# Performance work log

Measured on AMD Instinct MI355X. Metric: run time of the kernel, lower is better.

The kernel has to match this reference:

```python
import jax, jax.numpy as jnp
import numpy as np
from math import sqrt

NUM_HEADS = 16
NUM_KV_HEADS = 4
ROPE_BASE = 10000.0


def setup_inputs() -> dict:
    key = jax.random.key(0)
    ks = jax.random.split(key, 9)
    B, S, E = 4, 2048, 2048
    KV_DIM = NUM_KV_HEADS * (E // NUM_HEADS)  # 512
    s = 0.02
    return {
        "x": jax.random.normal(ks[0], (B, S, E), jnp.float32),
        "wq": jax.random.normal(ks[1], (E, E), jnp.float32) * s,
        "bq": jnp.zeros((E,), jnp.float32),
        "wk": jax.random.normal(ks[2], (KV_DIM, E), jnp.float32) * s,
        "bk": jnp.zeros((KV_DIM,), jnp.float32),
        "wv": jax.random.normal(ks[3], (KV_DIM, E), jnp.float32) * s,
        "bv": jnp.zeros((KV_DIM,), jnp.float32),
        "wo": jax.random.normal(ks[4], (E, E), jnp.float32) * s,
        "bo": jnp.zeros((E,), jnp.float32),
    }


def _rope_cos_sin(seq_len, head_dim, dtype):
    inv_freq = 1.0 / (ROPE_BASE ** (jnp.arange(0, head_dim, 2, dtype=jnp.float32) / head_dim))
    pos = jnp.arange(seq_len, dtype=jnp.float32)
    freqs = pos[:, None] * inv_freq[None, :]            # [S, D/2]
    emb = jnp.concatenate([freqs, freqs], axis=-1)      # [S, D]
    return jnp.cos(emb).astype(dtype), jnp.sin(emb).astype(dtype)


def _apply_rope(t, cos, sin):
    # t: [B, H, S, D]; cos/sin: [S, D]
    d2 = t.shape[-1] // 2
    rot = jnp.concatenate([-t[..., d2:], t[..., :d2]], axis=-1)
    return t * cos[None, None, :, :] + rot * sin[None, None, :, :]


def reference(x, wq, bq, wk, bk, wv, bv, wo, bo):
    B, S, E = x.shape
    H, KV = NUM_HEADS, NUM_KV_HEADS
    D = E // H
    G = H // KV

    q = (x @ wq.T + bq).reshape(B, S, H, D).transpose(0, 2, 1, 3)   # [B,H,S,D]
    k = (x @ wk.T + bk).reshape(B, S, KV, D).transpose(0, 2, 1, 3)  # [B,KV,S,D]
    v = (x @ wv.T + bv).reshape(B, S, KV, D).transpose(0, 2, 1, 3)

    cos, sin = _rope_cos_sin(S, D, x.dtype)
    q = _apply_rope(q, cos, sin)
    k = _apply_rope(k, cos, sin)

    # GQA: expand each kv head group_size times (contiguous repeat)
    k = jnp.repeat(k, G, axis=1)  # [B,H,S,D]
    v = jnp.repeat(v, G, axis=1)

    scores = jnp.einsum("bhqd,bhkd->bhqk", q, k)
    causal = jnp.triu(jnp.ones((S, S), dtype=bool), k=1)
    scores = jnp.where(causal[None, None, :, :], -jnp.inf, scores)
    attn = jax.nn.softmax(scores / sqrt(D), axis=-1)
    out = jnp.einsum("bhqk,bhkd->bhqd", attn, v)        # [B,H,S,D]
    out = out.transpose(0, 2, 1, 3).reshape(B, S, E)
    return out @ wo.T + bo
```

## Files before the change

kernel.cpp:

```cpp
#include <hip/hip_runtime.h>
#include <stdint.h>
#include <math.h>

typedef __attribute__((ext_vector_type(8))) short s16x8;
typedef __attribute__((ext_vector_type(4))) short s16x4;
typedef __attribute__((ext_vector_type(4))) float f32x4;

#define NEGH (-1.0e30f)

__device__ __forceinline__ short f2bf(float f) {
  union { float f; unsigned int i; } c; c.f = f;
  unsigned int lsb = (c.i >> 16) & 1u;
  c.i += 0x7fffu + lsb;
  return (short)(c.i >> 16);
}
__device__ __forceinline__ float bf2f(short u) {
  union { unsigned int i; float f; } c;
  c.i = ((unsigned int)(unsigned short)u) << 16;
  return c.f;
}

#define GLOAD_LDS16(gp, lp)                                                  \
  __builtin_amdgcn_global_load_lds(                                          \
      (__attribute__((address_space(1))) void*)(void*)(gp),                  \
      (__attribute__((address_space(3))) void*)(lp), 16, 0, 0)

__global__ __launch_bounds__(256) void cvt_kernel(const float* __restrict__ in,
                                                  short* __restrict__ out)
{
  const size_t i = ((size_t)blockIdx.x * 256 + threadIdx.x) * 4;
  const float4 v = *(const float4*)(in + i);
  s16x4 o = { f2bf(v.x), f2bf(v.y), f2bf(v.z), f2bf(v.w) };
  *(s16x4*)(out + i) = o;
}

__global__ __launch_bounds__(256) void gemm_bt(
    const short* __restrict__ A, const short* __restrict__ W,
    const float* __restrict__ bias, void* __restrict__ C,
    int M, int N, int K, int omode)
{
  __shared__ __align__(16) short As[128 * 64];
  __shared__ __align__(16) short Bs[128 * 64];

  const int t = threadIdx.x;
  const int l = t & 63;
  const int w = t >> 6;
  const int lane16 = l & 15;
  const int quad = l >> 4;
  const int wm = w >> 1, wn = w & 1;
  const int mb0 = blockIdx.y * 128;
  const int nb0 = blockIdx.x * 128;

  const f32x4 zero = {0.f, 0.f, 0.f, 0.f};
  f32x4 acc[4][4];
#pragma unroll
  for (int i = 0; i < 4; ++i)
#pragma unroll
    for (int j = 0; j < 4; ++j) acc[i][j] = zero;

  const int sr = t >> 3;
  const int sp = t & 7;
  const short* Ag = A + (size_t)(mb0 + sr) * K + sp * 8;
  const short* Wg = W + (size_t)(nb0 + sr) * K + sp * 8;
  short* Al = As + t * 8;
  short* Bl = Bs + t * 8;

  const int nkt = K >> 6;
  for (int kt = 0; kt < nkt; ++kt) {
    __syncthreads();
    const int kof = kt * 64;
#pragma unroll
    for (int it = 0; it < 4; ++it) {
      GLOAD_LDS16(Ag + kof + (size_t)(it * 32) * K, Al + it * 2048);
      GLOAD_LDS16(Wg + kof + (size_t)(it * 32) * K, Bl + it * 2048);
    }
    __syncthreads();
#pragma unroll
    for (int kk = 0; kk < 2; ++kk) {
      s16x8 af[4], bf[4];
#pragma unroll
      for (int mi = 0; mi < 4; ++mi)
        af[mi] = *(const s16x8*)&As[(wm * 64 + mi * 16 + lane16) * 64 +
                                    kk * 32 + quad * 8];
#pragma unroll
      for (int ni = 0; ni < 4; ++ni)
        bf[ni] = *(const s16x8*)&Bs[(wn * 64 + ni * 16 + lane16) * 64 +
                                    kk * 32 + quad * 8];
#pragma unroll
      for (int mi = 0; mi < 4; ++mi)
#pragma unroll
        for (int ni = 0; ni < 4; ++ni)
          acc[mi][ni] = __builtin_amdgcn_mfma_f32_16x16x32_bf16(
              af[mi], bf[ni], acc[mi][ni], 0, 0, 0);
    }
  }

#pragma unroll
  for (int ni = 0; ni < 4; ++ni) {
    const int n = nb0 + wn * 64 + ni * 16 + lane16;
    const float bv = bias[n];
#pragma unroll
    for (int mi = 0; mi < 4; ++mi) {
      const int m0 = mb0 + wm * 64 + mi * 16 + quad * 4;
#pragma unroll
      for (int r = 0; r < 4; ++r) {
        const int m = m0 + r;
        const float v = acc[mi][ni][r] + bv;
        if (omode == 0) {
          ((short*)C)[(size_t)m * N + n] = f2bf(v);
        } else if (omode == 1) {
          ((float*)C)[(size_t)m * N + n] = v;
        } else {
          ((short*)C)[((size_t)(m >> 11) * N + n) * 2048 + (m & 2047)] = f2bf(v);
        }
      }
    }
  }
}

__global__ __launch_bounds__(512, 2) void gemm256_bt(
    const short* __restrict__ A, const short* __restrict__ W,
    const float* __restrict__ bias, void* __restrict__ C,
    int M, int N, int K, int omode)
{
  __shared__ __align__(16) short Asm[2 * 16384];
  __shared__ __align__(16) short Bsm[2 * 16384];

  const int t = threadIdx.x;
  const int l = t & 63;
  const int w = t >> 6;
  const int lane16 = l & 15;
  const int quad = l >> 4;
  const int wm = w >> 2;
  const int wn = w & 3;
  const int mb0 = blockIdx.y * 256;
  const int nb0 = blockIdx.x * 256;

  const f32x4 zero = {0.f, 0.f, 0.f, 0.f};
  f32x4 acc[8][4];
#pragma unroll
  for (int i = 0; i < 8; ++i)
#pragma unroll
    for (int j = 0; j < 4; ++j) acc[i][j] = zero;

  const int srow = t >> 2;
  const int scs = (t & 3) ^ ((t >> 3) & 3);
  const short* Ag = A + (size_t)(mb0 + srow) * K + scs * 8;
  const short* Wg = W + (size_t)(nb0 + srow) * K + scs * 8;
  const size_t rstep = (size_t)128 * K;

#define STAGE_A(b, kt, kh)                                                    \
  do {                                                                        \
    const size_t ko_ = (size_t)(kt) * 64 + (kh) * 32;                         \
    GLOAD_LDS16(Ag + ko_,         Asm + (b) * 16384 + (kh) * 8192 + t * 8);   \
    GLOAD_LDS16(Ag + ko_ + rstep, Asm + (b) * 16384 + (kh) * 8192 + 4096 + t * 8); \
  } while (0)
#define STAGE_B(b, kt, kh)                                                    \
  do {                                                                        \
    const size_t ko_ = (size_t)(kt) * 64 + (kh) * 32;                         \
    GLOAD_LDS16(Wg + ko_,         Bsm + (b) * 16384 + (kh) * 8192 + t * 8);   \
    GLOAD_LDS16(Wg + ko_ + rstep, Bsm + (b) * 16384 + (kh) * 8192 + 4096 + t * 8); \
  } while (0)

  s16x8 bfr[4];

#define DO_PHASE(BUF, KK, MG, READB, STAGE_STMT, DO_VM)                       \
  {                                                                           \
    const short* Abase = Asm + (BUF) * 16384 + (KK) * 8192;                   \
    const short* Bbase = Bsm + (BUF) * 16384 + (KK) * 8192;                   \
    if (READB) {                                                              \
      _Pragma("unroll")                                                       \
      for (int ni = 0; ni < 4; ++ni) {                                        \
        const int nr = wn * 64 + ni * 16 + lane16;                            \
        bfr[ni] = *(const s16x8*)(Bbase + nr * 32 +                           \
                                  ((quad ^ ((nr >> 1) & 3)) << 3));           \
      }                                                                       \
    }                                                                         \
    s16x8 afr[4];                                                             \
    _Pragma("unroll")                                                         \
    for (int mi2 = 0; mi2 < 4; ++mi2) {                                       \
      const int mr = wm * 128 + (MG) * 64 + mi2 * 16 + lane16;                \
      afr[mi2] = *(const s16x8*)(Abase + mr * 32 +                            \
                                 ((quad ^ ((mr >> 1) & 3)) << 3));            \
    }                                                                         \
    STAGE_STMT;                                                               \
    __builtin_amdgcn_s_barrier();                                             \
    asm volatile("s_waitcnt lgkmcnt(0)" ::: "memory");                        \
    __builtin_amdgcn_sched_barrier(0);                                        \
    __builtin_amdgcn_s_setprio(1);                                            \
    _Pragma("unroll")                                                         \
    for (int mi2 = 0; mi2 < 4; ++mi2)                                         \
      _Pragma("unroll")                                                       \
      for (int ni = 0; ni < 4; ++ni)                                          \
        acc[(MG) * 4 + mi2][ni] = __builtin_amdgcn_mfma_f32_16x16x32_bf16(    \
            afr[mi2], bfr[ni], acc[(MG) * 4 + mi2][ni], 0, 0, 0);             \
    __builtin_amdgcn_s_setprio(0);                                            \
    if (DO_VM) {                                                              \
      asm volatile("s_waitcnt vmcnt(10)" ::: "memory");                       \
      __builtin_amdgcn_sched_barrier(0);                                      \
    }                                                                         \
    __builtin_amdgcn_s_barrier();                                             \
  }

  const int NT = K >> 6;

  STAGE_B(0, 0, 0); STAGE_A(0, 0, 0); STAGE_B(0, 0, 1); STAGE_A(0, 0, 1);
  STAGE_B(1, 1, 0); STAGE_A(1, 1, 0); STAGE_B(1, 1, 1);
  asm volatile("s_waitcnt vmcnt(10)" ::: "memory");
  __builtin_amdgcn_sched_barrier(0);
  __builtin_amdgcn_s_barrier();

  for (int i2 = 0; i2 < NT; i2 += 2) {
    const int tp1 = (i2 + 1 < NT) ? i2 + 1 : NT - 1;
    const int tp2 = (i2 + 2 < NT) ? i2 + 2 : NT - 1;
    const int tp3 = (i2 + 3 < NT) ? i2 + 3 : NT - 1;
    DO_PHASE(0, 0, 0, true,  STAGE_A(1, tp1, 1), false)
    DO_PHASE(0, 0, 1, false, STAGE_B(0, tp2, 0), true)
    DO_PHASE(0, 1, 0, true,  STAGE_A(0, tp2, 0), false)
    DO_PHASE(0, 1, 1, false, STAGE_B(0, tp2, 1), true)
    DO_PHASE(1, 0, 0, true,  STAGE_A(0, tp2, 1), false)
    DO_PHASE(1, 0, 1, false, STAGE_B(1, tp3, 0), true)
    DO_PHASE(1, 1, 0, true,  STAGE_A(1, tp3, 0), false)
    DO_PHASE(1, 1, 1, false, STAGE_B(1, tp3, 1), true)
  }

#pragma unroll
  for (int ni = 0; ni < 4; ++ni) {
    const int n = nb0 + wn * 64 + ni * 16 + lane16;
    const float bv = bias[n];
#pragma unroll
    for (int mi = 0; mi < 8; ++mi) {
      const int m0 = mb0 + wm * 128 + mi * 16 + quad * 4;
#pragma unroll
      for (int r = 0; r < 4; ++r) {
        const float v = acc[mi][ni][r] + bv;
        if (omode == 0) ((short*)C)[(size_t)(m0 + r) * N + n] = f2bf(v);
        else            ((float*)C)[(size_t)(m0 + r) * N + n] = v;
      }
    }
  }
#undef DO_PHASE
#undef STAGE_A
#undef STAGE_B
}

__global__ __launch_bounds__(256) void rope_kernel(short* __restrict__ buf,
                                                   int lognh)
{
  const int idx = blockIdx.x * 256 + threadIdx.x;
  const int d = idx & 63;
  const int rest = idx >> 6;
  const int row = rest >> lognh;
  const int pos = row & 2047;
  const float fr = (float)pos * exp2f((float)d * -0.20762050593048584f);
  float sn, cs;
  sincosf(fr, &sn, &cs);
  const size_t base = (size_t)rest * 128 + d;
  const float lo = bf2f(buf[base]);
  const float hi = bf2f(buf[base + 64]);
  buf[base]      = f2bf(lo * cs - hi * sn);
  buf[base + 64] = f2bf(hi * cs + lo * sn);
}

__global__ __launch_bounds__(512, 4) void attn_kernel(
    const short* __restrict__ qg, const short* __restrict__ kg,
    const short* __restrict__ vtg, short* __restrict__ og)
{
  __shared__ __align__(16) short Ksm[64 * 128];
  __shared__ __align__(16) short Vsm[128 * 64];
  __shared__ __align__(16) short Psm[128 * 64];

  const int t = threadIdx.x;
  const int l = t & 63;
  const int w = t >> 6;
  const int lane16 = l & 15;
  const int quad = l >> 4;
  const int jb = blockIdx.x;
  const int h = blockIdx.y, b = blockIdx.z;
  const int kv = h >> 2;

  const int krow = t >> 4, kseg = t & 15;
  const int vrow = t >> 3, vseg = t & 7;
  const int kswz = (kseg ^ (krow & 7)) * 8;
  const int vswz = (vseg ^ (vrow & 7)) * 8;

  const short* kbaseptr = kg + ((size_t)(b * 2048)) * 512 + kv * 128;
  const short* vbaseptr = vtg + ((size_t)(b * 512 + kv * 128)) * 2048;

  const float SC = 0.08838834764831845f * 1.4426950408889634f;
  const f32x4 zero = {0.f, 0.f, 0.f, 0.f};
  const int swz = (lane16 & 7) << 3;

  uint4 kr0, kr1, vr0, vr1;
#define LOADT(KB)                                                             \
  do {                                                                        \
    kr0 = *(const uint4*)(kbaseptr + (size_t)((KB) + krow) * 512 + kseg * 8); \
    kr1 = *(const uint4*)(kbaseptr + (size_t)((KB) + 32 + krow) * 512 + kseg * 8); \
    vr0 = *(const uint4*)(vbaseptr + (size_t)(vrow) * 2048 + (KB) + vseg * 8);     \
    vr1 = *(const uint4*)(vbaseptr + (size_t)(64 + vrow) * 2048 + (KB) + vseg * 8);\
  } while (0)
#define WRITET()                                                              \
  do {                                                                        \
    *(uint4*)&Ksm[krow * 128 + kswz] = kr0;                                   \
    *(uint4*)&Ksm[(32 + krow) * 128 + kswz] = kr1;                            \
    *(uint4*)&Vsm[vrow * 64 + vswz] = vr0;                                    \
    *(uint4*)&Vsm[(64 + vrow) * 64 + vswz] = vr1;                             \
  } while (0)

  for (int sp2 = 0; sp2 < 2; ++sp2) {
    const int jj = sp2 ? (15 - jb) : jb;
    const int qb0 = jj * 128;
    const int qw0 = qb0 + w * 16;
    const int qmaxw = qw0 + 15;
    const int ntl = 2 * jj + 2;

    s16x8 qf[4];
    {
      const short* qrow =
          qg + ((size_t)(b * 2048 + qw0 + lane16)) * 2048 + h * 128 + quad * 8;
#pragma unroll
      for (int kk = 0; kk < 4; ++kk) qf[kk] = *(const s16x8*)(qrow + kk * 32);
    }

    f32x4 o[8];
#pragma unroll
    for (int i = 0; i < 8; ++i) o[i] = zero;
    float m_i = NEGH, l_i = 0.f;

    LOADT(0);
    WRITET();

    for (int tl = 0; tl < ntl; ++tl) {
      __syncthreads();
      const int kbase = tl * 64;
      if (tl + 1 < ntl) LOADT((tl + 1) * 64);

      if (kbase <= qmaxw) {
        f32x4 st[4];
#pragma unroll
        for (int mt = 0; mt < 4; ++mt) st[mt] = zero;
#pragma unroll
        for (int mt = 0; mt < 4; ++mt) {
          const int rb = (mt * 16 + lane16) * 128;
#pragma unroll
          for (int kk = 0; kk < 4; ++kk) {
            const s16x8 a = *(const s16x8*)&Ksm[rb + ((kk * 32 + quad * 8) ^ swz)];
            st[mt] = __builtin_amdgcn_mfma_f32_16x16x32_bf16(a, qf[kk], st[mt], 0, 0, 0);
          }
        }

        const bool maskt = (kbase + 63 > qw0);
        const int qabs = qw0 + lane16;
        float tl_ = NEGH;
#pragma unroll
        for (int mt = 0; mt < 4; ++mt)
#pragma unroll
          for (int r = 0; r < 4; ++r) {
            float xx = st[mt][r] * SC;
            if (maskt && (kbase + mt * 16 + quad * 4 + r) > qabs) xx = NEGH;
            st[mt][r] = xx;
            tl_ = fmaxf(tl_, xx);
          }
        tl_ = fmaxf(tl_, __shfl_xor(tl_, 16));
        tl_ = fmaxf(tl_, __shfl_xor(tl_, 32));
        const float mnew = fmaxf(m_i, tl_);
        const float alpha = exp2f(m_i - mnew);
        float rs = 0.f;
#pragma unroll
        for (int mt = 0; mt < 4; ++mt) {
          const float p0 = exp2f(st[mt][0] - mnew);
          const float p1 = exp2f(st[mt][1] - mnew);
          const float p2 = exp2f(st[mt][2] - mnew);
          const float p3 = exp2f(st[mt][3] - mnew);
          rs += (p0 + p1) + (p2 + p3);
          s16x4 pk = { f2bf(p0), f2bf(p1), f2bf(p2), f2bf(p3) };
          *(s16x4*)&Psm[(w * 16 + lane16) * 64 + ((mt * 16 + quad * 4) ^ swz)] = pk;
        }
        rs += __shfl_xor(rs, 16);
        rs += __shfl_xor(rs, 32);
        l_i = l_i * alpha + rs;
        m_i = mnew;

#pragma unroll
        for (int r = 0; r < 4; ++r) {
          const float ar = __shfl(alpha, quad * 4 + r);
#pragma unroll
          for (int ntd = 0; ntd < 8; ++ntd) o[ntd][r] *= ar;
        }

        const int prb = (w * 16 + lane16) * 64;
#pragma unroll
        for (int kk = 0; kk < 2; ++kk) {
          const s16x8 pf = *(const s16x8*)&Psm[prb + ((kk * 32 + quad * 8) ^ swz)];
#pragma unroll
          for (int ntd = 0; ntd < 8; ++ntd) {
            const s16x8 vf =
                *(const s16x8*)&Vsm[(ntd * 16 + lane16) * 64 + ((kk * 32 + quad * 8) ^ swz)];
            o[ntd] = __builtin_amdgcn_mfma_f32_16x16x32_bf16(pf, vf, o[ntd], 0, 0, 0);
          }
        }
      }

      __syncthreads();
      if (tl + 1 < ntl) WRITET();
    }

#pragma unroll
    for (int r = 0; r < 4; ++r) {
      const float lr = __shfl(l_i, quad * 4 + r);
      const float inv = 1.f / lr;
      const size_t base =
          ((size_t)(b * 2048 + qw0 + quad * 4 + r)) * 2048 + h * 128 + lane16;
#pragma unroll
      for (int ntd = 0; ntd < 8; ++ntd) og[base + ntd * 16] = f2bf(o[ntd][r] * inv);
    }
  }
#undef LOADT
#undef WRITET
}

extern "C" void kernel_launch(void* const* d_in, const int* in_sizes, int n_in,
                              void* d_out, int out_size, void* d_ws,
                              size_t ws_size, hipStream_t stream)
{
  const float* x  = (const float*)d_in[0];
  const float* wq = (const float*)d_in[1];
  const float* bq = (const float*)d_in[2];
  const float* wk = (const float*)d_in[3];
  const float* bk = (const float*)d_in[4];
  const float* wv = (const float*)d_in[5];
  const float* bv = (const float*)d_in[6];
  const float* wo = (const float*)d_in[7];
  const float* bo = (const float*)d_in[8];
  float* out = (float*)d_out;

  char* ws = (char*)d_ws;
  short* xb  = (short*)ws;
  short* wqb = (short*)(ws + (32ull << 20));
  short* wkb = (short*)(ws + (40ull << 20));
  short* wvb = (short*)(ws + (42ull << 20));
  short* qws = (short*)(ws + (44ull << 20));
  short* wob = xb;
  short* kws = (short*)d_out;
  short* vtw = (short*)((char*)d_out + (8ull << 20));

  const dim3 blk(256);
  cvt_kernel<<<16384, blk, 0, stream>>>(x,  xb);
  cvt_kernel<<<4096,  blk, 0, stream>>>(wq, wqb);
  cvt_kernel<<<1024,  blk, 0, stream>>>(wk, wkb);
  cvt_kernel<<<1024,  blk, 0, stream>>>(wv, wvb);
  gemm256_bt<<<dim3(8, 32), dim3(512), 0, stream>>>(xb, wqb, bq, qws, 8192, 2048, 2048, 0);
  gemm_bt<<<dim3(4, 64),  blk, 0, stream>>>(xb, wkb, bk, kws, 8192, 512, 2048, 0);
  gemm_bt<<<dim3(4, 64),  blk, 0, stream>>>(xb, wvb, bv, vtw, 8192, 512, 2048, 2);
  rope_kernel<<<32768, blk, 0, stream>>>(qws, 4);
  rope_kernel<<<8192,  blk, 0, stream>>>(kws, 2);
  cvt_kernel<<<4096, blk, 0, stream>>>(wo, wob);
  attn_kernel<<<dim3(8, 16, 4), dim3(512), 0, stream>>>(qws, kws, vtw, qws);
  gemm256_bt<<<dim3(8, 32), dim3(512), 0, stream>>>(qws, wob, bo, out, 8192, 2048, 2048, 1);
}
```

Before: 565.2 us.

## Fuse K/V projections, tabulate RoPE, and streamline attention softmax

K and V projections now run as a single GEMM with N=1024, since wkb and wvb sit next to each other in the workspace. V is written row-major to a scratch buffer and then transposed by a new LDS-tiled kernel, replacing the old scattered transposed stores. RoPE cos/sin values are precomputed once into a table instead of calling sincosf per element. The attention inner loop also changes: it skips the causal-mask work on unmasked tiles, folds the softmax scale into an fma before exp2, skips output rescaling when the running max is unchanged, packs to bf16 with v_cvt_pk_bf16_f32, and raises wave priority around the MFMA sections with s_setprio.

```diff
diff --git a/kernel.cpp b/kernel.cpp
--- a/kernel.cpp
+++ b/kernel.cpp
@@ -36,7 +36,8 @@
 
 __global__ __launch_bounds__(256) void gemm_bt(
     const short* __restrict__ A, const short* __restrict__ W,
-    const float* __restrict__ bias, void* __restrict__ C,
+    const float* __restrict__ bias, const float* __restrict__ bias2,
+    void* __restrict__ C, void* __restrict__ C2,
     int M, int N, int K, int omode)
 {
   __shared__ __align__(16) short As[128 * 64];
@@ -98,20 +99,21 @@
 #pragma unroll
   for (int ni = 0; ni < 4; ++ni) {
     const int n = nb0 + wn * 64 + ni * 16 + lane16;
-    const float bv = bias[n];
+    const float bvx = (omode == 3 && n >= 512) ? bias2[n - 512] : bias[n];
 #pragma unroll
     for (int mi = 0; mi < 4; ++mi) {
       const int m0 = mb0 + wm * 64 + mi * 16 + quad * 4;
 #pragma unroll
       for (int r = 0; r < 4; ++r) {
         const int m = m0 + r;
-        const float v = acc[mi][ni][r] + bv;
+        const float v = acc[mi][ni][r] + bvx;
         if (omode == 0) {
           ((short*)C)[(size_t)m * N + n] = f2bf(v);
         } else if (omode == 1) {
           ((float*)C)[(size_t)m * N + n] = v;
         } else {
-          ((short*)C)[((size_t)(m >> 11) * N + n) * 2048 + (m & 2047)] = f2bf(v);
+          if (n < 512) ((short*)C)[(size_t)m * 512 + n] = f2bf(v);
+          else         ((short*)C2)[(size_t)m * 512 + (n - 512)] = f2bf(v);
         }
       }
     }
@@ -244,22 +246,58 @@
 #undef STAGE_B
 }
 
+__global__ __launch_bounds__(256) void rope_tab_kernel(float2* __restrict__ tab)
+{
+  const int i = blockIdx.x * 256 + threadIdx.x;
+  const int pos = i >> 6, d = i & 63;
+  const float fr = (float)pos * exp2f((float)d * -0.20762050593048584f);
+  float sn, cs;
+  sincosf(fr, &sn, &cs);
+  tab[i] = make_float2(cs, sn);
+}
+
 __global__ __launch_bounds__(256) void rope_kernel(short* __restrict__ buf,
-                                                   int lognh)
+                                                   int lognh,
+                                                   const float2* __restrict__ tab)
 {
   const int idx = blockIdx.x * 256 + threadIdx.x;
   const int d = idx & 63;
   const int rest = idx >> 6;
   const int row = rest >> lognh;
   const int pos = row & 2047;
-  const float fr = (float)pos * exp2f((float)d * -0.20762050593048584f);
-  float sn, cs;
-  sincosf(fr, &sn, &cs);
+  const float2 cssn = tab[(pos << 6) | d];
+  const float cs = cssn.x, sn = cssn.y;
   const size_t base = (size_t)rest * 128 + d;
   const float lo = bf2f(buf[base]);
   const float hi = bf2f(buf[base + 64]);
   buf[base]      = f2bf(lo * cs - hi * sn);
   buf[base + 64] = f2bf(hi * cs + lo * sn);
+}
+
+__global__ __launch_bounds__(256) void trans_kernel(const short* __restrict__ in,
+                                                    short* __restrict__ out)
+{
+  __shared__ short T[64 * 72];
+  const int t = threadIdx.x;
+  const int ms = blockIdx.x * 64;
+  const int ns = blockIdx.y * 64;
+  const int b = ms >> 11;
+  const int sl = ms & 2047;
+  const int r = t >> 3, sg = t & 7;
+#pragma unroll
+  for (int j = 0; j < 2; ++j) {
+    const uint4 v = *(const uint4*)(in + (size_t)(ms + r + 32 * j) * 512 + ns + sg * 8);
+    *(uint4*)&T[(r + 32 * j) * 72 + sg * 8] = v;
+  }
+  __syncthreads();
+#pragma unroll
+  for (int j = 0; j < 2; ++j) {
+    const int nr = r + 32 * j;
+    s16x8 v;
+#pragma unroll
+    for (int i = 0; i < 8; ++i) v[i] = T[(sg * 8 + i) * 72 + nr];
+    *(s16x8*)(out + ((size_t)(b * 512 + ns + nr)) * 2048 + sl + sg * 8) = v;
+  }
 }
 
 __global__ __launch_bounds__(512, 4) void attn_kernel(
@@ -339,6 +377,7 @@
         f32x4 st[4];
 #pragma unroll
         for (int mt = 0; mt < 4; ++mt) st[mt] = zero;
+        __builtin_amdgcn_s_setprio(1);
 #pragma unroll
         for (int mt = 0; mt < 4; ++mt) {
           const int rb = (mt * 16 + lane16) * 128;
@@ -348,47 +387,61 @@
             st[mt] = __builtin_amdgcn_mfma_f32_16x16x32_bf16(a, qf[kk], st[mt], 0, 0, 0);
           }
         }
+        __builtin_amdgcn_s_setprio(0);
 
         const bool maskt = (kbase + 63 > qw0);
         const int qabs = qw0 + lane16;
         float tl_ = NEGH;
-#pragma unroll
-        for (int mt = 0; mt < 4; ++mt)
-#pragma unroll
-          for (int r = 0; r < 4; ++r) {
-            float xx = st[mt][r] * SC;
-            if (maskt && (kbase + mt * 16 + quad * 4 + r) > qabs) xx = NEGH;
-            st[mt][r] = xx;
-            tl_ = fmaxf(tl_, xx);
-          }
+        if (maskt) {
+#pragma unroll
+          for (int mt = 0; mt < 4; ++mt)
+#pragma unroll
+            for (int r = 0; r < 4; ++r) {
+              float xx = st[mt][r];
+              if ((kbase + mt * 16 + quad * 4 + r) > qabs) xx = NEGH;
+              st[mt][r] = xx;
+              tl_ = fmaxf(tl_, xx);
+            }
+        } else {
+#pragma unroll
+          for (int mt = 0; mt < 4; ++mt)
+#pragma unroll
+            for (int r = 0; r < 4; ++r) tl_ = fmaxf(tl_, st[mt][r]);
+        }
         tl_ = fmaxf(tl_, __shfl_xor(tl_, 16));
         tl_ = fmaxf(tl_, __shfl_xor(tl_, 32));
         const float mnew = fmaxf(m_i, tl_);
-        const float alpha = exp2f(m_i - mnew);
+        if (!__all(tl_ <= m_i)) {
+          const float alpha = exp2f((m_i - mnew) * SC);
+          l_i *= alpha;
+#pragma unroll
+          for (int r = 0; r < 4; ++r) {
+            const float ar = __shfl(alpha, quad * 4 + r);
+#pragma unroll
+            for (int ntd = 0; ntd < 8; ++ntd) o[ntd][r] *= ar;
+          }
+        }
+        m_i = mnew;
+        const float mS = mnew * SC;
         float rs = 0.f;
 #pragma unroll
         for (int mt = 0; mt < 4; ++mt) {
-          const float p0 = exp2f(st[mt][0] - mnew);
-          const float p1 = exp2f(st[mt][1] - mnew);
-          const float p2 = exp2f(st[mt][2] - mnew);
-          const float p3 = exp2f(st[mt][3] - mnew);
+          const float p0 = exp2f(fmaf(st[mt][0], SC, -mS));
+          const float p1 = exp2f(fmaf(st[mt][1], SC, -mS));
+          const float p2 = exp2f(fmaf(st[mt][2], SC, -mS));
+          const float p3 = exp2f(fmaf(st[mt][3], SC, -mS));
           rs += (p0 + p1) + (p2 + p3);
-          s16x4 pk = { f2bf(p0), f2bf(p1), f2bf(p2), f2bf(p3) };
-          *(s16x4*)&Psm[(w * 16 + lane16) * 64 + ((mt * 16 + quad * 4) ^ swz)] = pk;
+          uint2 pk2;
+          asm("v_cvt_pk_bf16_f32 %0, %1, %2" : "=v"(pk2.x) : "v"(p0), "v"(p1));
+          asm("v_cvt_pk_bf16_f32 %0, %1, %2" : "=v"(pk2.y) : "v"(p2), "v"(p3));
+          *(uint2*)&Psm[(w * 16 + lane16) * 64 + ((mt * 16 + quad * 4) ^ swz)] = pk2;
         }
         rs += __shfl_xor(rs, 16);
         rs += __shfl_xor(rs, 32);
-        l_i = l_i * alpha + rs;
-        m_i = mnew;
-
-#pragma unroll
-        for (int r = 0; r < 4; ++r) {
-          const float ar = __shfl(alpha, quad * 4 + r);
-#pragma unroll
-          for (int ntd = 0; ntd < 8; ++ntd) o[ntd][r] *= ar;
-        }
+        l_i += rs;
 
         const int prb = (w * 16 + lane16) * 64;
+        __builtin_amdgcn_s_setprio(1);
 #pragma unroll
         for (int kk = 0; kk < 2; ++kk) {
           const s16x8 pf = *(const s16x8*)&Psm[prb + ((kk * 32 + quad * 8) ^ swz)];
@@ -399,6 +452,7 @@
             o[ntd] = __builtin_amdgcn_mfma_f32_16x16x32_bf16(pf, vf, o[ntd], 0, 0, 0);
           }
         }
+        __builtin_amdgcn_s_setprio(0);
       }
 
       __syncthreads();
@@ -440,20 +494,23 @@
   short* wkb = (short*)(ws + (40ull << 20));
   short* wvb = (short*)(ws + (42ull << 20));
   short* qws = (short*)(ws + (44ull << 20));
+  float2* tab = (float2*)(ws + (76ull << 20));
   short* wob = xb;
   short* kws = (short*)d_out;
   short* vtw = (short*)((char*)d_out + (8ull << 20));
+  short* vtmp = (short*)((char*)d_out + (16ull << 20));
 
   const dim3 blk(256);
   cvt_kernel<<<16384, blk, 0, stream>>>(x,  xb);
   cvt_kernel<<<4096,  blk, 0, stream>>>(wq, wqb);
   cvt_kernel<<<1024,  blk, 0, stream>>>(wk, wkb);
   cvt_kernel<<<1024,  blk, 0, stream>>>(wv, wvb);
+  rope_tab_kernel<<<512, blk, 0, stream>>>(tab);
   gemm256_bt<<<dim3(8, 32), dim3(512), 0, stream>>>(xb, wqb, bq, qws, 8192, 2048, 2048, 0);
-  gemm_bt<<<dim3(4, 64),  blk, 0, stream>>>(xb, wkb, bk, kws, 8192, 512, 2048, 0);
-  gemm_bt<<<dim3(4, 64),  blk, 0, stream>>>(xb, wvb, bv, vtw, 8192, 512, 2048, 2);
-  rope_kernel<<<32768, blk, 0, stream>>>(qws, 4);
-  rope_kernel<<<8192,  blk, 0, stream>>>(kws, 2);
+  gemm_bt<<<dim3(8, 64), blk, 0, stream>>>(xb, wkb, bk, bv, kws, vtmp, 8192, 1024, 2048, 3);
+  trans_kernel<<<dim3(128, 8), blk, 0, stream>>>(vtmp, vtw);
+  rope_kernel<<<32768, blk, 0, stream>>>(qws, 4, tab);
+  rope_kernel<<<8192,  blk, 0, stream>>>(kws, 2, tab);
   cvt_kernel<<<4096, blk, 0, stream>>>(wo, wob);
   attn_kernel<<<dim3(8, 16, 4), dim3(512), 0, stream>>>(qws, kws, vtw, qws);
   gemm256_bt<<<dim3(8, 32), dim3(512), 0, stream>>>(qws, wob, bo, out, 8192, 2048, 2048, 1);
```

Measured after the change: 532.8 us. -5.7%, faster.
